# Kernel tuning notes

Measured on AMD Instinct MI355X. Metric: run time of the kernel, lower is better.

## Reference

```python
import jax, jax.numpy as jnp
import numpy as np

FP8_MAX = 448.0  # torch.finfo(torch.float8_e4m3fn).max
FP8_MIN = -448.0


def per_tensor_quantize(t):
    # amax = max(|min|, |max|) over the whole tensor
    amax = jnp.maximum(jnp.abs(jnp.min(t)), jnp.abs(jnp.max(t)))
    scale = FP8_MAX / jnp.clip(amax, 1e-12, None)
    q = jnp.clip(t * scale, FP8_MIN, FP8_MAX).astype(jnp.float8_e4m3fn)
    inv_scale = (1.0 / scale).astype(jnp.float32)
    return q, inv_scale


def setup_inputs() -> dict:
    key = jax.random.key(0)
    k1, k2 = jax.random.split(key)
    B, S, D_IN, D_OUT = 8, 8192, 1024, 1024
    x = jax.random.normal(k1, (B, S, D_IN), dtype=jnp.float32)
    w = jax.random.normal(k2, (D_OUT, D_IN), dtype=jnp.float32) * 0.02
    qweight, weight_scale = per_tensor_quantize(w)  # fp8 weight + scalar fp32 scale
    return {"x": x, "qweight": qweight, "weight_scale": weight_scale}


def reference(x, qweight, weight_scale):
    # dynamic per-tensor activation quantization (quantize -> fp8)
    qinput, act_scale = per_tensor_quantize(x)
    # fp8 gemm with inline dequant scales (manual dequant-linear path, bias=None)
    A = qinput.astype(x.dtype) * act_scale          # [B, S, D_in]
    W = qweight.astype(x.dtype) * weight_scale.astype(x.dtype)  # [D_out, D_in]
    out = jnp.einsum('bsk,nk->bsn', A, W)           # [B, S, D_out]
    return out
```

## Files before the change

### kernel.cpp

```cpp
#include <hip/hip_runtime.h>
#include <hip/hip_fp8.h>
#include <stdint.h>
#include <cmath>

using f32x4  = __attribute__((ext_vector_type(4)))  float;
using f32x16 = __attribute__((ext_vector_type(16))) float;
using i32x4  = __attribute__((ext_vector_type(4)))  int;
using i32x8  = __attribute__((ext_vector_type(8)))  int;

#define FP8MAX 448.0f

__device__ __forceinline__ uint8_t to_fp8(float v) {
  __hip_fp8_e4m3 q(fminf(fmaxf(v, -FP8MAX), FP8MAX));
  return q.__x;
}

__device__ __forceinline__ uint32_t quant4(float4 v, float s) {
  return (uint32_t)to_fp8(v.x * s) | ((uint32_t)to_fp8(v.y * s) << 8) |
         ((uint32_t)to_fp8(v.z * s) << 16) | ((uint32_t)to_fp8(v.w * s) << 24);
}

__global__ void amax_wconv(const float* __restrict__ x, size_t n4,
                           unsigned int* __restrict__ amax_u,
                           const uint8_t* __restrict__ w,
                           uint8_t* __restrict__ qw, int n1) {
  if ((int)blockIdx.x * 1024 < n1) {
    const float* wf = (const float*)w;
    const unsigned short* wh = (const unsigned short*)w;
    int f32ok = 1, bf16ok = 1;
    for (int i = threadIdx.x; i < 4096; i += 256) {
      float v = wf[i];
      if (!(isfinite(v) && fabsf(v) <= FP8MAX)) f32ok = 0;
      else { __hip_fp8_e4m3 qq(v); if ((float)qq != v) f32ok = 0; }
      float hv = __uint_as_float(((unsigned int)wh[i]) << 16);
      if (!(isfinite(hv) && fabsf(hv) <= FP8MAX)) bf16ok = 0;
      else { __hip_fp8_e4m3 qh(hv); if ((float)qh != hv) bf16ok = 0; }
    }
    __shared__ int sf, sb;
    if (threadIdx.x == 0) { sf = 1; sb = 1; }
    __syncthreads();
    if (!f32ok) atomicAnd(&sf, 0);
    if (!bf16ok) atomicAnd(&sb, 0);
    __syncthreads();
    unsigned int f = sf ? 2u : (sb ? 1u : 0u);

    int i0 = (blockIdx.x * 256 + threadIdx.x) * 4;
    if (i0 < n1) {
      uint32_t out;
      if (f == 2) {
        float4 v = *(const float4*)((const float*)w + i0);
        out = (uint32_t)to_fp8(v.x) | ((uint32_t)to_fp8(v.y) << 8) |
              ((uint32_t)to_fp8(v.z) << 16) | ((uint32_t)to_fp8(v.w) << 24);
      } else if (f == 1) {
        ushort4 h = *(const ushort4*)((const unsigned short*)w + i0);
        out = (uint32_t)to_fp8(__uint_as_float(((unsigned int)h.x) << 16)) |
              ((uint32_t)to_fp8(__uint_as_float(((unsigned int)h.y) << 16)) << 8) |
              ((uint32_t)to_fp8(__uint_as_float(((unsigned int)h.z) << 16)) << 16) |
              ((uint32_t)to_fp8(__uint_as_float(((unsigned int)h.w) << 16)) << 24);
      } else {
        out = *(const uint32_t*)(w + i0);
      }
      *(uint32_t*)(qw + i0) = out;
    }
  }

  const float4* x4 = (const float4*)x;
  float m = 0.0f;
  size_t stride = (size_t)gridDim.x * blockDim.x;
  for (size_t i = (size_t)blockIdx.x * blockDim.x + threadIdx.x; i < n4; i += stride) {
    float4 v = x4[i];
    m = fmaxf(m, fmaxf(fmaxf(fabsf(v.x), fabsf(v.y)),
                       fmaxf(fabsf(v.z), fabsf(v.w))));
  }
  #pragma unroll
  for (int off = 32; off > 0; off >>= 1)
    m = fmaxf(m, __shfl_xor(m, off));
  __shared__ float sm[16];
  int wid = threadIdx.x >> 6;
  if ((threadIdx.x & 63) == 0) sm[wid] = m;
  __syncthreads();
  if (threadIdx.x == 0) {
    int nw = blockDim.x >> 6;
    float r = sm[0];
    for (int i = 1; i < nw; i++) r = fmaxf(r, sm[i]);
    atomicMax(amax_u, __float_as_uint(r));
  }
}

#define SROWS 64

__global__ __launch_bounds__(256, 2) void fused_gemm(
    const float* __restrict__ X,
    const uint8_t* __restrict__ B,
    float* __restrict__ C,
    const float* __restrict__ amax_p,
    const float* __restrict__ wscale_p) {
  __shared__ uint8_t qa[SROWS * 1024];

  const int t = threadIdx.x;
  const int lane = t & 63;
  const int wave = t >> 6;

  const float amax = fmaxf(amax_p[0], 1e-12f);
  const float scale = FP8MAX / amax;
  const float s = (1.0f / scale) * wscale_p[0];

  const float4* x4 = (const float4*)(X + (size_t)blockIdx.x * (SROWS * 1024));
  #pragma unroll 4
  for (int i = 0; i < 64; ++i) {
    float4 v = x4[i * 256 + t];
    uint32_t wq = quant4(v, scale);
    int swc = (t >> 2) ^ (i & 15);
    *(uint32_t*)&qa[i * 1024 + swc * 16 + (t & 3) * 4] = wq;
  }
  __syncthreads();

  const int lr = lane & 31;
  const int kh = lane >> 5;
  const int x15 = lr & 15;

  const uint8_t* bbase = B + (size_t)(wave * 64 + lr) * 1024 + kh * 32;

  const size_t c_row0 = (size_t)blockIdx.x * SROWS;

  auto loadB = [&](int ss, i32x8* bf) {
    const uint8_t* p = bbase + (size_t)(ss >> 4) * (256 * 1024) + (ss & 15) * 64;
    #pragma unroll
    for (int j = 0; j < 2; j++) {
      const uint8_t* q = p + (size_t)j * (32 * 1024);
      i32x4 lo = *(const i32x4*)q;
      i32x4 hi = *(const i32x4*)(q + 16);
      bf[j] = (i32x8){lo.x, lo.y, lo.z, lo.w, hi.x, hi.y, hi.z, hi.w};
    }
  };
  auto loadA = [&](int ss, i32x8* af) {
    int cb = (ss & 15) * 4 + kh * 2;
    #pragma unroll
    for (int i = 0; i < 2; i++) {
      const uint8_t* p = &qa[(i * 32 + lr) * 1024];
      i32x4 lo = *(const i32x4*)(p + ((cb    ) ^ x15) * 16);
      i32x4 hi = *(const i32x4*)(p + ((cb + 1) ^ x15) * 16);
      af[i] = (i32x8){lo.x, lo.y, lo.z, lo.w, hi.x, hi.y, hi.z, hi.w};
    }
  };

  f32x16 acc[2][2] = {};
  i32x8 a0[2], b0[2], a1[2], b1[2];
  loadA(0, a0); loadB(0, b0);

  for (int ss = 0; ss < 64; ss += 2) {
    loadA(ss + 1, a1); loadB(ss + 1, b1);
    __builtin_amdgcn_s_setprio(1);
    #pragma unroll
    for (int i = 0; i < 2; i++)
      #pragma unroll
      for (int j = 0; j < 2; j++)
        acc[i][j] = __builtin_amdgcn_mfma_scale_f32_32x32x64_f8f6f4(
            a0[i], b0[j], acc[i][j], 0, 0, 0, 0x7f7f7f7f, 0, 0x7f7f7f7f);
    __builtin_amdgcn_s_setprio(0);

    int s2 = (ss + 2 < 64) ? ss + 2 : 63;
    loadA(s2, a0); loadB(s2, b0);
    __builtin_amdgcn_s_setprio(1);
    #pragma unroll
    for (int i = 0; i < 2; i++)
      #pragma unroll
      for (int j = 0; j < 2; j++)
        acc[i][j] = __builtin_amdgcn_mfma_scale_f32_32x32x64_f8f6f4(
            a1[i], b1[j], acc[i][j], 0, 0, 0, 0x7f7f7f7f, 0, 0x7f7f7f7f);
    __builtin_amdgcn_s_setprio(0);

    if (((ss + 1) & 15) == 15) {
      int n = ss >> 4;
      #pragma unroll
      for (int i = 0; i < 2; i++) {
        #pragma unroll
        for (int j = 0; j < 2; j++) {
          size_t row0 = c_row0 + i * 32 + (kh << 2);
          int col = n * 256 + wave * 64 + j * 32 + lr;
          #pragma unroll
          for (int r = 0; r < 16; r++) {
            size_t row = row0 + (r & 3) + ((r >> 2) << 3);
            C[row * 1024 + col] = acc[i][j][r] * s;
          }
          acc[i][j] = (f32x16)(0.0f);
        }
      }
    }
  }
}

extern "C" void kernel_launch(void* const* d_in, const int* in_sizes, int n_in,
                              void* d_out, int out_size, void* d_ws, size_t ws_size,
                              hipStream_t stream) {
  const float* x = (const float*)d_in[0];
  const uint8_t* wraw = (const uint8_t*)d_in[1];
  const float* wscale = (const float*)d_in[2];
  float* out = (float*)d_out;

  long long in0 = in_sizes[0];
  long long in1 = in_sizes[1];
  double kd = sqrt((double)in0 * (double)in1 / (double)out_size);
  long long K = (long long)(kd + 0.5);
  long long M = in0 / K;

  unsigned int* amax_u = (unsigned int*)d_ws;
  const float* amax_f = (const float*)d_ws;
  uint8_t* qw = (uint8_t*)d_ws + 4096;

  hipMemsetAsync(d_ws, 0, 4, stream);
  amax_wconv<<<2048, 256, 0, stream>>>(x, (size_t)(in0 / 4), amax_u,
                                       wraw, qw, (int)in1);
  fused_gemm<<<(unsigned)(M / SROWS), 256, 0, stream>>>(x, qw, out,
                                                        amax_f, wscale);
}
```

Before: 256.2 us.

## Deepen B-fragment prefetch to four stages and reverse strip order for cache reuse

Restructures the GEMM inner loop so B fragments are prefetched four k-steps ahead from global memory, while A fragments from LDS are double-buffered one step ahead. This hides more global load latency behind the MFMA work. Blocks now process row strips in reverse order, so the tail of X that the amax kernel just read is likely still cached when the GEMM starts. The quantize loop unroll goes from 4 to 8. The extra in-flight fragments raise register pressure, which could limit occupancy under the two-blocks-per-CU launch bound.

```diff
diff --git a/kernel.cpp b/kernel.cpp
--- a/kernel.cpp
+++ b/kernel.cpp
@@ -94,9 +94,11 @@
     const uint8_t* __restrict__ B,
     float* __restrict__ C,
     const float* __restrict__ amax_p,
-    const float* __restrict__ wscale_p) {
+    const float* __restrict__ wscale_p,
+    int nstrips) {
   __shared__ uint8_t qa[SROWS * 1024];
 
+  const int strip = nstrips - 1 - (int)blockIdx.x;
   const int t = threadIdx.x;
   const int lane = t & 63;
   const int wave = t >> 6;
@@ -105,9 +107,9 @@
   const float scale = FP8MAX / amax;
   const float s = (1.0f / scale) * wscale_p[0];
 
-  const float4* x4 = (const float4*)(X + (size_t)blockIdx.x * (SROWS * 1024));
-  #pragma unroll 4
-  for (int i = 0; i < 64; ++i) {
+  const float4* x4 = (const float4*)(X + (size_t)strip * (SROWS * 1024));
+  #pragma unroll 8
+  for (int i = 0; i < SROWS; ++i) {
     float4 v = x4[i * 256 + t];
     uint32_t wq = quant4(v, scale);
     int swc = (t >> 2) ^ (i & 15);
@@ -121,7 +123,7 @@
 
   const uint8_t* bbase = B + (size_t)(wave * 64 + lr) * 1024 + kh * 32;
 
-  const size_t c_row0 = (size_t)blockIdx.x * SROWS;
+  const size_t c_row0 = (size_t)strip * SROWS;
 
   auto loadB = [&](int ss, i32x8* bf) {
     const uint8_t* p = bbase + (size_t)(ss >> 4) * (256 * 1024) + (ss & 15) * 64;
@@ -145,33 +147,35 @@
   };
 
   f32x16 acc[2][2] = {};
-  i32x8 a0[2], b0[2], a1[2], b1[2];
-  loadA(0, a0); loadB(0, b0);
-
-  for (int ss = 0; ss < 64; ss += 2) {
-    loadA(ss + 1, a1); loadB(ss + 1, b1);
-    __builtin_amdgcn_s_setprio(1);
-    #pragma unroll
-    for (int i = 0; i < 2; i++)
-      #pragma unroll
-      for (int j = 0; j < 2; j++)
-        acc[i][j] = __builtin_amdgcn_mfma_scale_f32_32x32x64_f8f6f4(
-            a0[i], b0[j], acc[i][j], 0, 0, 0, 0x7f7f7f7f, 0, 0x7f7f7f7f);
-    __builtin_amdgcn_s_setprio(0);
-
-    int s2 = (ss + 2 < 64) ? ss + 2 : 63;
-    loadA(s2, a0); loadB(s2, b0);
-    __builtin_amdgcn_s_setprio(1);
-    #pragma unroll
-    for (int i = 0; i < 2; i++)
-      #pragma unroll
-      for (int j = 0; j < 2; j++)
-        acc[i][j] = __builtin_amdgcn_mfma_scale_f32_32x32x64_f8f6f4(
-            a1[i], b1[j], acc[i][j], 0, 0, 0, 0x7f7f7f7f, 0, 0x7f7f7f7f);
-    __builtin_amdgcn_s_setprio(0);
-
-    if (((ss + 1) & 15) == 15) {
-      int n = ss >> 4;
+  i32x8 bs0[2], bs1[2], bs2[2], bs3[2];
+  i32x8 as0[2], as1[2];
+
+  loadB(0, bs0); loadB(1, bs1); loadB(2, bs2); loadB(3, bs3);
+  loadA(0, as0);
+
+  #define GSTEP(SS, ACUR, ANXT, BSET)                                        \
+    {                                                                        \
+      const int ss_ = (SS);                                                  \
+      loadA(ss_ + 1 < 64 ? ss_ + 1 : 63, ANXT);                              \
+      __builtin_amdgcn_s_setprio(1);                                         \
+      _Pragma("unroll")                                                      \
+      for (int i = 0; i < 2; i++)                                            \
+        _Pragma("unroll")                                                    \
+        for (int j = 0; j < 2; j++)                                          \
+          acc[i][j] = __builtin_amdgcn_mfma_scale_f32_32x32x64_f8f6f4(       \
+              ACUR[i], BSET[j], acc[i][j], 0, 0, 0, 0x7f7f7f7f, 0, 0x7f7f7f7f); \
+      __builtin_amdgcn_s_setprio(0);                                         \
+      loadB(ss_ + 4 < 64 ? ss_ + 4 : 63, BSET);                              \
+    }
+
+  for (int base = 0; base < 64; base += 4) {
+    GSTEP(base + 0, as0, as1, bs0);
+    GSTEP(base + 1, as1, as0, bs1);
+    GSTEP(base + 2, as0, as1, bs2);
+    GSTEP(base + 3, as1, as0, bs3);
+
+    if ((base & 15) == 12) {
+      int n = base >> 4;
       #pragma unroll
       for (int i = 0; i < 2; i++) {
         #pragma unroll
@@ -188,6 +192,7 @@
       }
     }
   }
+  #undef GSTEP
 }
 
 extern "C" void kernel_launch(void* const* d_in, const int* in_sizes, int n_in,
@@ -203,6 +208,7 @@
   double kd = sqrt((double)in0 * (double)in1 / (double)out_size);
   long long K = (long long)(kd + 0.5);
   long long M = in0 / K;
+  int nstrips = (int)(M / SROWS);
 
   unsigned int* amax_u = (unsigned int*)d_ws;
   const float* amax_f = (const float*)d_ws;
@@ -211,6 +217,6 @@
   hipMemsetAsync(d_ws, 0, 4, stream);
   amax_wconv<<<2048, 256, 0, stream>>>(x, (size_t)(in0 / 4), amax_u,
                                        wraw, qw, (int)in1);
-  fused_gemm<<<(unsigned)(M / SROWS), 256, 0, stream>>>(x, qw, out,
-                                                        amax_f, wscale);
-}
+  fused_gemm<<<(unsigned)nstrips, 256, 0, stream>>>(x, qw, out,
+                                                    amax_f, wscale, nstrips);
+}
```

Result: no change. 253.6 us (-1.0%).
